# Kernel tuning notes

Hardware: AMD Instinct MI355X
Metric: run time of the kernel (lower is better)

The kernel has to match this reference:

```python
import jax, jax.numpy as jnp
import numpy as np

# ---- DMP constants (from DMPParameters with N=5, tau=1, dt=1/(T*l), Dof=9, a_z=25) ----
N_BASIS = 5
T_STEPS = 10
L_SUB = 10
DIM = 9                      # len(state_index)
TAU = 1.0
DT = TAU / (T_STEPS * L_SUB)            # 0.01
TIME_STEPS = int(round(TAU / DT)) + 1   # 101
A_X = 1.0
A_Z = 25.0
B_Z = A_Z / 4.0
_c_np = np.exp(-A_X * np.linspace(0.0, 1.0, N_BASIS))
C = jnp.asarray(_c_np, dtype=jnp.float32)                          # rbf centers
H = jnp.asarray(N_BASIS ** 1.5 / _c_np / A_X, dtype=jnp.float32)   # rbf widths (sigma2)


def _integrate(w, y0, dy0, goal):
    """Euler integration of the DMP dynamical system.
    w: (R, N) basis weights; y0, dy0, goal: (R,) with R = batch*DIM.
    Returns Y: (R, TIME_STEPS) positions."""
    scale = goal - y0  # fixed forcing-term scaling

    def step(carry, _):
        y, z, x = carry
        x = x + (-A_X * x / TAU) * DT                  # canonical system
        psi = jnp.exp(-H * (x - C) ** 2)               # (N,) gaussian rbf
        fx = (w @ psi) * x * scale / jnp.sum(psi)      # (R,) forcing term
        dz = (A_Z * (B_Z * (goal - y) - z) + fx) / TAU
        dy = z / TAU
        y = y + dy * DT
        z = z + dz * DT
        return (y, z, x), y

    z0 = dy0 * TAU
    _, ys = jax.lax.scan(step, (y0, z0, jnp.float32(1.0)), None, length=TIME_STEPS - 1)
    # prepend initial position, transpose to (R, TIME_STEPS)
    return jnp.concatenate([y0[None, :], ys], axis=0).T


def setup_inputs():
    key = jax.random.key(0)
    ks = jax.random.split(key, 4)
    B, D_IN, HID = 16384, 128, 2048
    out_size = DIM * (N_BASIS + 1)  # 54 = N*dim + dim
    return {
        "input": jax.random.normal(ks[0], (B, D_IN), jnp.float32),
        "W0": jax.random.normal(ks[1], (HID, D_IN), jnp.float32) / np.sqrt(D_IN),
        "b0": jnp.full((HID,), 0.1, jnp.float32),
        "W1": jax.random.normal(ks[2], (HID, HID), jnp.float32) / np.sqrt(HID),
        "b1": jnp.full((HID,), 0.1, jnp.float32),
        "Wl": jax.random.normal(ks[3], (out_size, HID), jnp.float32) / np.sqrt(HID),
        "bl": jnp.zeros((out_size,), jnp.float32),
    }


def reference(input, W0, b0, W1, b1, Wl, bl):
    B = input.shape[0]
    # MLP backbone with tanh hidden activation
    h = jnp.tanh(input @ W0.T + b0)
    h = jnp.tanh(h @ W1.T + b1)
    out = (h @ Wl.T + bl) * 100.0                          # (B, DIM*(N+1))
    # split DMP parameters: goal then basis weights
    goal = out[:, :DIM].reshape(-1)                        # (B*DIM,)
    w = out[:, DIM:DIM * (N_BASIS + 1)].reshape(-1, N_BASIS)  # (B*DIM, N)
    y0 = input[:, 7:16].reshape(-1)                        # state_index
    dy0 = input[:, 22:31].reshape(-1)                      # vel_index
    Y = _integrate(w, y0, dy0, goal)                       # (B*DIM, 101)
    y = Y.reshape(B, DIM, TIME_STEPS)[:, :, ::L_SUB]       # (B, DIM, T+1)
    return y[:, :, 1:] - y[:, :, :-1]                      # (B, DIM, T)
```

## Files before the change

### kernel.cpp

```cpp
#include <hip/hip_runtime.h>
#include <hip/hip_fp16.h>
#include <math.h>

typedef _Float16 f16;
typedef _Float16 f16x8 __attribute__((ext_vector_type(8)));
typedef _Float16 f16x4v __attribute__((ext_vector_type(4)));
typedef float f32x4 __attribute__((ext_vector_type(4)));

#define B_SZ 16384
#define D_INP 128
#define HID 2048
#define DIMS 9
#define OUTC 54
#define OUTP 64

__device__ __forceinline__ void load_lds16(const f16* g, f16* l) {
    __builtin_amdgcn_global_load_lds(
        (__attribute__((address_space(1))) void*)(g),
        (__attribute__((address_space(3))) void*)(l),
        16, 0, 0);
}

__device__ __forceinline__ float fast_tanh(float x) {
    float e = __builtin_amdgcn_exp2f(2.885390081777927f * x);
    return 1.0f - 2.0f * __builtin_amdgcn_rcpf(e + 1.0f);
}

#define N4_INP (B_SZ * D_INP / 4)
#define N4_W0  (HID * D_INP / 4)
#define N4_W1  (HID * HID / 4)
#define N4_WL  (OUTP * HID / 4)
__global__ __launch_bounds__(256) void cvt_fused_kernel(
    const float* __restrict__ input, const float* __restrict__ W0,
    const float* __restrict__ W1, const float* __restrict__ Wl,
    f16* __restrict__ inp16, f16* __restrict__ w0q,
    f16* __restrict__ w1q, f16* __restrict__ wlq)
{
    int i = blockIdx.x * 256 + threadIdx.x;
    const float* s; f16* d; int j;
    if (i < N4_INP) { s = input; d = inp16; j = i; }
    else if (i < N4_INP + N4_W0) { s = W0; d = w0q; j = i - N4_INP; }
    else if (i < N4_INP + N4_W0 + N4_W1) { s = W1; d = w1q; j = i - N4_INP - N4_W0; }
    else {
        j = i - N4_INP - N4_W0 - N4_W1;
        int e0 = j * 4, row = e0 >> 11, col = e0 & (HID - 1);
        f16x4v o;
        if (row < OUTC) {
            float4 v = ((const float4*)Wl)[(row * HID + col) >> 2];
            o.x = (f16)v.x; o.y = (f16)v.y; o.z = (f16)v.z; o.w = (f16)v.w;
        } else {
            o.x = (f16)0.f; o.y = (f16)0.f; o.z = (f16)0.f; o.w = (f16)0.f;
        }
        ((f16x4v*)wlq)[j] = o;
        return;
    }
    float4 v = ((const float4*)s)[j];
    f16x4v o;
    o.x = (f16)v.x; o.y = (f16)v.y; o.z = (f16)v.z; o.w = (f16)v.w;
    ((f16x4v*)d)[j] = o;
}

template <int BN, int EPI>
__global__ __launch_bounds__(256, 2) void gemm_nt(
    const f16* __restrict__ A, const f16* __restrict__ Bm,
    const float* __restrict__ bias, void* __restrict__ Cout,
    int M, int N, int K, int bias_n)
{
    constexpr int BM = 128, BK = 32;
    constexpr int NI = BN / 32;
    __shared__ __align__(16) f16 sa[BM * BK];
    __shared__ __align__(16) f16 sb[BN * BK];

    const int tid  = threadIdx.x;
    const int lane = tid & 63;
    const int wave = tid >> 6;
    const int wm = wave >> 1, wn = wave & 1;
    const int m0 = blockIdx.x * BM;
    const int n0 = blockIdx.y * BN;

    const int k_len = K / gridDim.z;
    const int k_beg = blockIdx.z * k_len;
    const int k_end = k_beg + k_len;

    f32x4 acc[4][NI];
    #pragma unroll
    for (int i = 0; i < 4; ++i)
        #pragma unroll
        for (int j = 0; j < NI; ++j) acc[i][j] = (f32x4){0.f, 0.f, 0.f, 0.f};

    const int r_a = lane >> 2;
    const int kk  = (((lane & 3) ^ ((lane >> 3) & 3)) << 3);
    const int swz = (lane >> 1) & 3;

    for (int k0 = k_beg; k0 < k_end; k0 += BK) {
        #pragma unroll
        for (int c = 0; c < (BM * BK * 2) / 4096; ++c) {
            int o = c * 4096 + wave * 1024;
            const f16* gp = A + (size_t)(m0 + (o >> 6) + r_a) * K + k0 + kk;
            load_lds16(gp, (f16*)((char*)sa + o));
        }
        #pragma unroll
        for (int c = 0; c < (BN * BK * 2) / 4096; ++c) {
            int o = c * 4096 + wave * 1024;
            const f16* gp = Bm + (size_t)(n0 + (o >> 6) + r_a) * K + k0 + kk;
            load_lds16(gp, (f16*)((char*)sb + o));
        }
        __syncthreads();

        f16x8 af[4], bf[NI];
        const int csA = ((lane >> 4) ^ swz) * 8;
        #pragma unroll
        for (int mi = 0; mi < 4; ++mi)
            af[mi] = *(const f16x8*)&sa[(wm * 64 + mi * 16 + (lane & 15)) * BK + csA];
        #pragma unroll
        for (int ni = 0; ni < NI; ++ni)
            bf[ni] = *(const f16x8*)&sb[(wn * (BN / 2) + ni * 16 + (lane & 15)) * BK + csA];
        #pragma unroll
        for (int mi = 0; mi < 4; ++mi)
            #pragma unroll
            for (int ni = 0; ni < NI; ++ni)
                acc[mi][ni] = __builtin_amdgcn_mfma_f32_16x16x32_f16(af[mi], bf[ni], acc[mi][ni], 0, 0, 0);
        __syncthreads();
    }

    const int crow0 = m0 + wm * 64 + (lane >> 4) * 4;
    const int ccol0 = n0 + wn * (BN / 2) + (lane & 15);
    if (EPI == 0) {
        f16* C = (f16*)Cout;
        #pragma unroll
        for (int mi = 0; mi < 4; ++mi)
            #pragma unroll
            for (int ni = 0; ni < NI; ++ni) {
                int col = ccol0 + ni * 16;
                float bv = bias[col];
                #pragma unroll
                for (int r2 = 0; r2 < 4; ++r2) {
                    float v = fast_tanh(acc[mi][ni][r2] + bv);
                    C[(size_t)(crow0 + mi * 16 + r2) * N + col] = (f16)v;
                }
            }
    } else {
        float* C = (float*)Cout;
        #pragma unroll
        for (int mi = 0; mi < 4; ++mi)
            #pragma unroll
            for (int ni = 0; ni < NI; ++ni) {
                int col = ccol0 + ni * 16;
                float bv = (blockIdx.z == 0 && col < bias_n) ? bias[col] * 100.0f : 0.0f;
                #pragma unroll
                for (int r2 = 0; r2 < 4; ++r2) {
                    float v = acc[mi][ni][r2] * 100.0f + bv;
                    atomicAdd(&C[(size_t)(crow0 + mi * 16 + r2) * N + col], v);
                }
            }
    }
}

__global__ __launch_bounds__(256) void integrate_kernel(
    const float* __restrict__ out3, const float* __restrict__ input,
    float* __restrict__ out)
{
    __shared__ float g[500];
    {
        int k = threadIdx.x;
        if (k < 100) {
            float x = expf(-0.010050335853501441f * (float)(k + 1));
            float psi[5], ssum = 0.0f;
            #pragma unroll
            for (int n = 0; n < 5; ++n) {
                float c = expf(-0.25f * (float)n);
                float h = 11.180339887498949f / c;
                float dx = x - c;
                psi[n] = expf(-h * dx * dx);
                ssum += psi[n];
            }
            float inv = x / ssum;
            #pragma unroll
            for (int n = 0; n < 5; ++n) g[k * 5 + n] = psi[n] * inv;
        }
    }
    __syncthreads();

    int r = blockIdx.x * 256 + threadIdx.x;
    int b = r / DIMS, d = r - b * DIMS;

    const float* ob = out3 + (size_t)b * OUTP;
    float goal = ob[d];
    float w0 = ob[DIMS + d * 5 + 0];
    float w1 = ob[DIMS + d * 5 + 1];
    float w2 = ob[DIMS + d * 5 + 2];
    float w3 = ob[DIMS + d * 5 + 3];
    float w4 = ob[DIMS + d * 5 + 4];

    float y = input[(size_t)b * D_INP + 7 + d];
    float z = input[(size_t)b * D_INP + 22 + d];
    const float scale = goal - y;

    float prev = y;
    float* op = out + (size_t)b * (DIMS * 10) + d * 10;
    int j = 0;
    for (int k = 0; k < 100; ++k) {
        const float* gk = &g[k * 5];
        float fx = scale * (w0 * gk[0] + w1 * gk[1] + w2 * gk[2] + w3 * gk[3] + w4 * gk[4]);
        float dz = 25.0f * (6.25f * (goal - y) - z) + fx;
        y = y + z * 0.01f;
        z = z + dz * 0.01f;
        if ((k % 10) == 9) { op[j] = y - prev; prev = y; ++j; }
    }
}

extern "C" void kernel_launch(void* const* d_in, const int* in_sizes, int n_in,
                              void* d_out, int out_size, void* d_ws, size_t ws_size,
                              hipStream_t stream) {
    (void)in_sizes; (void)n_in; (void)out_size; (void)ws_size;
    const float* input = (const float*)d_in[0];
    const float* W0 = (const float*)d_in[1];
    const float* b0 = (const float*)d_in[2];
    const float* W1 = (const float*)d_in[3];
    const float* b1 = (const float*)d_in[4];
    const float* Wl = (const float*)d_in[5];
    const float* bl = (const float*)d_in[6];
    float* out = (float*)d_out;

    f16* inp16 = (f16*)d_ws;
    f16* w0q = inp16 + (size_t)B_SZ * D_INP;
    f16* w1q = w0q + (size_t)HID * D_INP;
    f16* wlq = w1q + (size_t)HID * HID;
    f16* h1  = wlq + (size_t)OUTP * HID;
    f16* h2  = h1 + (size_t)B_SZ * HID;
    float* out3 = (float*)(h2 + (size_t)B_SZ * HID);

    int n4_total = N4_INP + N4_W0 + N4_W1 + N4_WL;
    cvt_fused_kernel<<<(n4_total + 255) / 256, 256, 0, stream>>>(
        input, W0, W1, Wl, inp16, w0q, w1q, wlq);
    hipMemsetAsync(out3, 0, (size_t)B_SZ * OUTP * sizeof(float), stream);

    gemm_nt<128, 0><<<dim3(B_SZ / 128, HID / 128, 1), 256, 0, stream>>>(
        inp16, w0q, b0, (void*)h1, B_SZ, HID, D_INP, HID);
    gemm_nt<128, 0><<<dim3(B_SZ / 128, HID / 128, 1), 256, 0, stream>>>(
        h1, w1q, b1, (void*)h2, B_SZ, HID, HID, HID);
    gemm_nt<64, 1><<<dim3(B_SZ / 128, 1, 8), 256, 0, stream>>>(
        h2, wlq, bl, (void*)out3, B_SZ, OUTP, HID, OUTC);

    integrate_kernel<<<B_SZ * DIMS / 256, 256, 0, stream>>>(out3, input, out);
}
```

Baseline: 314.3 us.

## Double GEMM K-tile with new LDS swizzle; replace split-K atomics with partial buffers

Raises the GEMM K tile from 32 to 64 and uses a row-XOR swizzle over 8 column groups, so each barrier pair covers two MFMA k-chunks and there are half as many sync and load rounds. The final small GEMM now writes split-K partials (4 slices instead of 8) to separate buffers that reuse the h1 workspace, rather than atomically adding into a zeroed buffer. The integrate kernel sums the partials, which removes the memset and the atomic traffic. The larger K tile doubles LDS use per block, which may lower occupancy.

```diff
diff --git a/kernel.cpp b/kernel.cpp
--- a/kernel.cpp
+++ b/kernel.cpp
@@ -13,6 +13,7 @@
 #define DIMS 9
 #define OUTC 54
 #define OUTP 64
+#define NZ3 4
 
 __device__ __forceinline__ void load_lds16(const f16* g, f16* l) {
     __builtin_amdgcn_global_load_lds(
@@ -66,7 +67,7 @@
     const float* __restrict__ bias, void* __restrict__ Cout,
     int M, int N, int K, int bias_n)
 {
-    constexpr int BM = 128, BK = 32;
+    constexpr int BM = 128, BK = 64;
     constexpr int NI = BN / 32;
     __shared__ __align__(16) f16 sa[BM * BK];
     __shared__ __align__(16) f16 sb[BN * BK];
@@ -88,38 +89,43 @@
         #pragma unroll
         for (int j = 0; j < NI; ++j) acc[i][j] = (f32x4){0.f, 0.f, 0.f, 0.f};
 
-    const int r_a = lane >> 2;
-    const int kk  = (((lane & 3) ^ ((lane >> 3) & 3)) << 3);
-    const int swz = (lane >> 1) & 3;
+    const int r8 = lane >> 3;
+    const int cg = (((lane & 7) ^ r8) << 3);
 
     for (int k0 = k_beg; k0 < k_end; k0 += BK) {
         #pragma unroll
         for (int c = 0; c < (BM * BK * 2) / 4096; ++c) {
             int o = c * 4096 + wave * 1024;
-            const f16* gp = A + (size_t)(m0 + (o >> 6) + r_a) * K + k0 + kk;
+            const f16* gp = A + (size_t)(m0 + (o >> 7) + r8) * K + k0 + cg;
             load_lds16(gp, (f16*)((char*)sa + o));
         }
         #pragma unroll
         for (int c = 0; c < (BN * BK * 2) / 4096; ++c) {
             int o = c * 4096 + wave * 1024;
-            const f16* gp = Bm + (size_t)(n0 + (o >> 6) + r_a) * K + k0 + kk;
+            const f16* gp = Bm + (size_t)(n0 + (o >> 7) + r8) * K + k0 + cg;
             load_lds16(gp, (f16*)((char*)sb + o));
         }
         __syncthreads();
 
-        f16x8 af[4], bf[NI];
-        const int csA = ((lane >> 4) ^ swz) * 8;
-        #pragma unroll
-        for (int mi = 0; mi < 4; ++mi)
-            af[mi] = *(const f16x8*)&sa[(wm * 64 + mi * 16 + (lane & 15)) * BK + csA];
-        #pragma unroll
-        for (int ni = 0; ni < NI; ++ni)
-            bf[ni] = *(const f16x8*)&sb[(wn * (BN / 2) + ni * 16 + (lane & 15)) * BK + csA];
-        #pragma unroll
-        for (int mi = 0; mi < 4; ++mi)
-            #pragma unroll
-            for (int ni = 0; ni < NI; ++ni)
-                acc[mi][ni] = __builtin_amdgcn_mfma_f32_16x16x32_f16(af[mi], bf[ni], acc[mi][ni], 0, 0, 0);
+        #pragma unroll
+        for (int kc = 0; kc < 2; ++kc) {
+            f16x8 af[4], bf[NI];
+            #pragma unroll
+            for (int mi = 0; mi < 4; ++mi) {
+                int ar = wm * 64 + mi * 16 + (lane & 15);
+                af[mi] = *(const f16x8*)&sa[ar * 64 + ((((kc << 2) | (lane >> 4)) ^ (ar & 7)) << 3)];
+            }
+            #pragma unroll
+            for (int ni = 0; ni < NI; ++ni) {
+                int br = wn * (BN / 2) + ni * 16 + (lane & 15);
+                bf[ni] = *(const f16x8*)&sb[br * 64 + ((((kc << 2) | (lane >> 4)) ^ (br & 7)) << 3)];
+            }
+            #pragma unroll
+            for (int mi = 0; mi < 4; ++mi)
+                #pragma unroll
+                for (int ni = 0; ni < NI; ++ni)
+                    acc[mi][ni] = __builtin_amdgcn_mfma_f32_16x16x32_f16(af[mi], bf[ni], acc[mi][ni], 0, 0, 0);
+        }
         __syncthreads();
     }
 
@@ -140,7 +146,7 @@
                 }
             }
     } else {
-        float* C = (float*)Cout;
+        float* C = (float*)Cout + (size_t)blockIdx.z * M * N;
         #pragma unroll
         for (int mi = 0; mi < 4; ++mi)
             #pragma unroll
@@ -150,14 +156,14 @@
                 #pragma unroll
                 for (int r2 = 0; r2 < 4; ++r2) {
                     float v = acc[mi][ni][r2] * 100.0f + bv;
-                    atomicAdd(&C[(size_t)(crow0 + mi * 16 + r2) * N + col], v);
+                    C[(size_t)(crow0 + mi * 16 + r2) * N + col] = v;
                 }
             }
     }
 }
 
 __global__ __launch_bounds__(256) void integrate_kernel(
-    const float* __restrict__ out3, const float* __restrict__ input,
+    const float* __restrict__ out3p, const float* __restrict__ input,
     float* __restrict__ out)
 {
     __shared__ float g[500];
@@ -184,13 +190,17 @@
     int r = blockIdx.x * 256 + threadIdx.x;
     int b = r / DIMS, d = r - b * DIMS;
 
-    const float* ob = out3 + (size_t)b * OUTP;
-    float goal = ob[d];
-    float w0 = ob[DIMS + d * 5 + 0];
-    float w1 = ob[DIMS + d * 5 + 1];
-    float w2 = ob[DIMS + d * 5 + 2];
-    float w3 = ob[DIMS + d * 5 + 3];
-    float w4 = ob[DIMS + d * 5 + 4];
+    float goal = 0.f, w0 = 0.f, w1 = 0.f, w2 = 0.f, w3 = 0.f, w4 = 0.f;
+    #pragma unroll
+    for (int z = 0; z < NZ3; ++z) {
+        const float* ob = out3p + (size_t)z * B_SZ * OUTP + (size_t)b * OUTP;
+        goal += ob[d];
+        w0 += ob[DIMS + d * 5 + 0];
+        w1 += ob[DIMS + d * 5 + 1];
+        w2 += ob[DIMS + d * 5 + 2];
+        w3 += ob[DIMS + d * 5 + 3];
+        w4 += ob[DIMS + d * 5 + 4];
+    }
 
     float y = input[(size_t)b * D_INP + 7 + d];
     float z = input[(size_t)b * D_INP + 22 + d];
@@ -228,19 +238,18 @@
     f16* wlq = w1q + (size_t)HID * HID;
     f16* h1  = wlq + (size_t)OUTP * HID;
     f16* h2  = h1 + (size_t)B_SZ * HID;
-    float* out3 = (float*)(h2 + (size_t)B_SZ * HID);
+    float* out3p = (float*)h1;
 
     int n4_total = N4_INP + N4_W0 + N4_W1 + N4_WL;
     cvt_fused_kernel<<<(n4_total + 255) / 256, 256, 0, stream>>>(
         input, W0, W1, Wl, inp16, w0q, w1q, wlq);
-    hipMemsetAsync(out3, 0, (size_t)B_SZ * OUTP * sizeof(float), stream);
 
     gemm_nt<128, 0><<<dim3(B_SZ / 128, HID / 128, 1), 256, 0, stream>>>(
         inp16, w0q, b0, (void*)h1, B_SZ, HID, D_INP, HID);
     gemm_nt<128, 0><<<dim3(B_SZ / 128, HID / 128, 1), 256, 0, stream>>>(
         h1, w1q, b1, (void*)h2, B_SZ, HID, HID, HID);
-    gemm_nt<64, 1><<<dim3(B_SZ / 128, 1, 8), 256, 0, stream>>>(
-        h2, wlq, bl, (void*)out3, B_SZ, OUTP, HID, OUTC);
-
-    integrate_kernel<<<B_SZ * DIMS / 256, 256, 0, stream>>>(out3, input, out);
-}
+    gemm_nt<64, 1><<<dim3(B_SZ / 128, 1, NZ3), 256, 0, stream>>>(
+        h2, wlq, bl, (void*)out3p, B_SZ, OUTP, HID, OUTC);
+
+    integrate_kernel<<<B_SZ * DIMS / 256, 256, 0, stream>>>(out3p, input, out);
+}
```

Result: faster. 270.8 us (-13.8%).
